# Performance work log

Measured on AMD Instinct MI355X. Metric: run time of the kernel, lower is better.

## Reference

```python
import jax, jax.numpy as jnp
import numpy as np

S = 64.0
MARGIN = 0.5

def setup_inputs() -> dict:
    key = jax.random.key(0)
    k1, k2 = jax.random.split(key)
    B, C = 256, 100000
    # cosine similarities in (-0.99, 0.99) so arccos is well-conditioned
    logits = jax.random.uniform(k1, (B, C), dtype=jnp.float32, minval=-0.99, maxval=0.99)
    labels = jax.random.randint(k2, (B,), 0, C, dtype=jnp.int64)
    return {"logits": logits, "labels": labels}

def _arcface(logits, labels):
    B = logits.shape[0]
    valid = labels != -1                     # rows with a real target
    safe_labels = jnp.where(valid, labels, 0)
    rows = jnp.arange(B)
    target = logits[rows, safe_labels]       # [B] target cosines
    # original does arccos over the whole matrix then cos back; off-target
    # entries reduce to identity, targets become cos(arccos(x) + m)
    new_target = jnp.cos(jnp.arccos(target) + MARGIN)
    new_target = jnp.where(valid, new_target, target)
    modified = logits.at[rows, safe_labels].set(new_target)
    # the no_grad block + custom Function make backward exactly grad * s
    return S * (logits + jax.lax.stop_gradient(modified - logits))

def reference(logits, labels):
    return _arcface(logits, labels)
```

## Files before the change

kernel.cpp:

```cpp
#include <hip/hip_runtime.h>
#include <hip/hip_bf16.h>
#include <math.h>


#define ARC_S      64.0f
#define COS_M      0.8775825618903728f
#define SIN_M      0.4794255386042030f

typedef float floatx4 __attribute__((ext_vector_type(4)));

__global__ __launch_bounds__(256) void arcface_kernel(
    const float* __restrict__ logits,
    const int*   __restrict__ labels,
    float*       __restrict__ out,
    int C, int C4, int strideV)
{
    const int row = blockIdx.y;
    const int lbl = labels[row];
    const size_t rowOff = (size_t)row * (size_t)C;
    const floatx4* __restrict__ in4  = (const floatx4*)(logits + rowOff);
    floatx4*       __restrict__ out4 = (floatx4*)(out + rowOff);

    int i4 = blockIdx.x * blockDim.x + threadIdx.x;

    #pragma unroll 4
    for (; i4 < C4; i4 += strideV) {
        floatx4 v = in4[i4];
        const int d = lbl - i4 * 4;
        if (d >= 0 && d < 4) {
            const float t = v[d];
            const float s = sqrtf(fmaxf(0.0f, 1.0f - t * t));
            v[d] = t * COS_M - s * SIN_M;
        }
        v *= ARC_S;
        __builtin_nontemporal_store(v, &out4[i4]);
    }
}

extern "C" void kernel_launch(void* const* d_in, const int* in_sizes, int n_in,
                              void* d_out, int out_size, void* d_ws, size_t ws_size,
                              hipStream_t stream) {
    const float* logits = (const float*)d_in[0];
    const int*   labels = (const int*)d_in[1];
    float*       out    = (float*)d_out;

    const int B = in_sizes[1];
    const int C = in_sizes[0] / B;
    const int C4 = C / 4;

    const int ITERS = 4;
    const int threads = 256;
    const int gridX = (C4 + threads * ITERS - 1) / (threads * ITERS);
    const int strideV = gridX * threads;

    dim3 block(threads, 1, 1);
    dim3 grid(gridX, B, 1);
    arcface_kernel<<<grid, block, 0, stream>>>(logits, labels, out, C, C4, strideV);
}
```

Measured before the change: 180.6 us.

## Split into flat vectorized scale-copy kernel plus single-block label fixup kernel

Replaces the per-row 2D grid with a flat streaming kernel where each thread issues eight 16-byte loads before storing, removing the per-element label check from the bulk loop. A second one-block kernel rewrites the target entries and handles the tail that does not fill a full 2048-vector chunk. This aims for more memory-level parallelism and simpler bulk code, at the cost of an extra launch and a serial dependency. The fixup kernel only covers rows up to 256 with one thread each.

```diff
diff --git a/kernel.cpp b/kernel.cpp
--- a/kernel.cpp
+++ b/kernel.cpp
@@ -9,32 +9,44 @@
 
 typedef float floatx4 __attribute__((ext_vector_type(4)));
 
-__global__ __launch_bounds__(256) void arcface_kernel(
+__global__ __launch_bounds__(256) void scale_copy_kernel(
+    const floatx4* __restrict__ in,
+    floatx4*       __restrict__ out)
+{
+    const size_t base = (size_t)blockIdx.x * 2048u + threadIdx.x;
+
+    floatx4 v[8];
+    #pragma unroll
+    for (int j = 0; j < 8; ++j)
+        v[j] = in[base + j * 256];
+
+    #pragma unroll
+    for (int j = 0; j < 8; ++j) {
+        floatx4 w = v[j] * ARC_S;
+        __builtin_nontemporal_store(w, &out[base + j * 256]);
+    }
+}
+
+__global__ __launch_bounds__(256) void fixup_kernel(
     const float* __restrict__ logits,
     const int*   __restrict__ labels,
     float*       __restrict__ out,
-    int C, int C4, int strideV)
+    int B, int C, size_t tailStart, size_t total)
 {
-    const int row = blockIdx.y;
-    const int lbl = labels[row];
-    const size_t rowOff = (size_t)row * (size_t)C;
-    const floatx4* __restrict__ in4  = (const floatx4*)(logits + rowOff);
-    floatx4*       __restrict__ out4 = (floatx4*)(out + rowOff);
+    const int t = threadIdx.x;
 
-    int i4 = blockIdx.x * blockDim.x + threadIdx.x;
+    if (t < B) {
+        const int lbl = labels[t];
+        if (lbl >= 0 && lbl < C) {
+            const size_t idx = (size_t)t * (size_t)C + (size_t)lbl;
+            const float x = logits[idx];
+            const float s = sqrtf(fmaxf(0.0f, 1.0f - x * x));
+            out[idx] = ARC_S * (x * COS_M - s * SIN_M);
+        }
+    }
 
-    #pragma unroll 4
-    for (; i4 < C4; i4 += strideV) {
-        floatx4 v = in4[i4];
-        const int d = lbl - i4 * 4;
-        if (d >= 0 && d < 4) {
-            const float t = v[d];
-            const float s = sqrtf(fmaxf(0.0f, 1.0f - t * t));
-            v[d] = t * COS_M - s * SIN_M;
-        }
-        v *= ARC_S;
-        __builtin_nontemporal_store(v, &out4[i4]);
-    }
+    for (size_t i = tailStart + t; i < total; i += 256)
+        out[i] = ARC_S * logits[i];
 }
 
 extern "C" void kernel_launch(void* const* d_in, const int* in_sizes, int n_in,
@@ -46,14 +58,13 @@
 
     const int B = in_sizes[1];
     const int C = in_sizes[0] / B;
-    const int C4 = C / 4;
+    const size_t total  = (size_t)B * (size_t)C;
+    const size_t total4 = total / 4;
+    const int    nChunks = (int)(total4 / 2048);
+    const size_t tailStart = (size_t)nChunks * 2048u * 4u;
 
-    const int ITERS = 4;
-    const int threads = 256;
-    const int gridX = (C4 + threads * ITERS - 1) / (threads * ITERS);
-    const int strideV = gridX * threads;
-
-    dim3 block(threads, 1, 1);
-    dim3 grid(gridX, B, 1);
-    arcface_kernel<<<grid, block, 0, stream>>>(logits, labels, out, C, C4, strideV);
+    scale_copy_kernel<<<dim3(nChunks), dim3(256), 0, stream>>>(
+        (const floatx4*)logits, (floatx4*)out);
+    fixup_kernel<<<dim3(1), dim3(256), 0, stream>>>(
+        logits, labels, out, B, C, tailStart, total);
 }
```

Measured after the change: 179.7 us. Within noise of the previous version (-0.5%).
